# Kernel tuning notes

Hardware: AMD Instinct MI355X
Metric: run time of the kernel (lower is better)

Reference implementation:

```python
import jax, jax.numpy as jnp
import numpy as np

B, L, DIM = 4, 2048, 512
H, D = 8, 64
SCALE = D ** -0.5
NEG = -10000.0


def setup_inputs() -> dict:
    key = jax.random.key(0)
    ks = jax.random.split(key, 5)
    std = 1.0 / np.sqrt(DIM)
    return {
        "x": jax.random.normal(ks[0], (B, L, DIM), dtype=jnp.float32),
        "wq": jax.random.normal(ks[1], (H * D, DIM), dtype=jnp.float32) * std,
        "wk": jax.random.normal(ks[2], (H * D, DIM), dtype=jnp.float32) * std,
        "wv": jax.random.normal(ks[3], (H * D, DIM), dtype=jnp.float32) * std,
        "wo": jax.random.normal(ks[4], (DIM, H * D), dtype=jnp.float32) * std,
    }


def reference(x, wq, wk, wv, wo):
    b, l, _ = x.shape
    # projections (torch Linear: y = x @ W.T), split heads -> [b,h,l,d]
    q = (x @ wq.T).reshape(b, l, H, D).transpose(0, 2, 1, 3)
    k = (x @ wk.T).reshape(b, l, H, D).transpose(0, 2, 1, 3)
    v = (x @ wv.T).reshape(b, l, H, D).transpose(0, 2, 1, 3)
    scores = jnp.einsum("bhld,bhsd->bhls", q, k) * SCALE
    scores = jnp.nan_to_num(scores, nan=0.0, posinf=10000.0, neginf=NEG)
    diag = jnp.eye(l, dtype=bool)[None, None]  # [1,1,l,l]
    scores = jnp.where(diag, NEG, scores)
    attn = jax.nn.softmax(scores, axis=-1)
    attn = jnp.where(diag, 0.0, attn)
    attn = jnp.nan_to_num(attn, nan=0.0, posinf=0.0, neginf=0.0)
    out = jnp.einsum("bhls,bhsd->bhld", attn, v)
    out = out.transpose(0, 2, 1, 3).reshape(b, l, H * D)
    return out @ wo.T
```

## Files before the change

kernel.cpp:

```cpp
#include <hip/hip_runtime.h>
#include <hip/hip_bf16.h>


#define Bsz 4
#define Lsz 2048
#define DIMsz 512
#define Hsz 8
#define Dsz 64

typedef _Float16 f16;
typedef __attribute__((ext_vector_type(8))) _Float16 f16x8;
typedef __attribute__((ext_vector_type(4))) _Float16 f16x4;
typedef __attribute__((ext_vector_type(2))) __fp16 fp16x2;
typedef __attribute__((ext_vector_type(4))) float f32x4;
typedef unsigned int u32;

#if __has_builtin(__builtin_amdgcn_exp2f)
#define EXP2(x) __builtin_amdgcn_exp2f(x)
#else
#define EXP2(x) __expf(0.6931471805599453f * (x))
#endif

__device__ __forceinline__ u32 pack2(float a, float b) {
#if __has_builtin(__builtin_amdgcn_cvt_pkrtz)
    fp16x2 h = __builtin_amdgcn_cvt_pkrtz(a, b);
    return __builtin_bit_cast(u32, h);
#else
    fp16x2 h; h.x = (__fp16)a; h.y = (__fp16)b;
    return __builtin_bit_cast(u32, h);
#endif
}

__device__ __forceinline__ void gl2lds16(const void* g, void* l) {
    __builtin_amdgcn_global_load_lds(
        (const __attribute__((address_space(1))) u32*)g,
        (__attribute__((address_space(3))) u32*)l, 16, 0, 0);
}

__global__ __launch_bounds__(256) void pack_f16(
    const float* __restrict__ x, const float* __restrict__ wq,
    const float* __restrict__ wk, const float* __restrict__ wv,
    const float* __restrict__ wo,
    f16* __restrict__ xh, f16* __restrict__ w3h, f16* __restrict__ woh)
{
    const int seg = blockIdx.y;
    const float* s; f16* d; int n; float sc = 1.0f;
    switch (seg) {
        case 0: s = x;  d = xh;            n = 4194304; break;
        case 1: s = wq; d = w3h;           n = 262144; sc = 0.18033688011112042f; break;
        case 2: s = wk; d = w3h + 262144;  n = 262144; break;
        case 3: s = wv; d = w3h + 524288;  n = 262144; break;
        default: s = wo; d = woh;          n = 262144; break;
    }
    int i = (blockIdx.x * 256 + threadIdx.x) * 4;
    if (i >= n) return;
    float4 v = *(const float4*)(s + i);
    f16x4 o;
    o.x = (f16)(v.x * sc); o.y = (f16)(v.y * sc);
    o.z = (f16)(v.z * sc); o.w = (f16)(v.w * sc);
    *(f16x4*)(d + i) = o;
}

__global__ __launch_bounds__(256) void gemm_qkv_f16(
    const f16* __restrict__ A, const f16* __restrict__ B,
    f16* __restrict__ qh, f16* __restrict__ kh, f16* __restrict__ vth)
{
    __shared__ __align__(16) char smem[17408];
    f16* Ash = (f16*)smem;
    f16* Bsh = (f16*)(smem + 8192);

    const int tid = threadIdx.x;
    const int w = tid >> 6, lane = tid & 63;
    const int quad = lane >> 4, low = lane & 15;
    const int wm = w >> 1, wn = w & 1;
    const int m0 = blockIdx.y * 128, n0 = blockIdx.x * 128;

    f32x4 acc[4][4];
    #pragma unroll
    for (int i = 0; i < 4; i++)
        #pragma unroll
        for (int j = 0; j < 4; j++) acc[i][j] = (f32x4){0.f, 0.f, 0.f, 0.f};

    #pragma unroll 1
    for (int k0 = 0; k0 < DIMsz; k0 += 32) {
        __syncthreads();
        #pragma unroll
        for (int j = 0; j < 2; j++) {
            int t = j * 256 + tid;
            int r = t >> 2, g = t & 3;
            int gc = (g ^ ((r >> 1) & 3)) * 8;
            char* lb = (char*)Ash + (j * 256 + w * 64) * 16;
            gl2lds16(A + (size_t)(m0 + r) * DIMsz + k0 + gc, lb);
            char* lb2 = (char*)Bsh + (j * 256 + w * 64) * 16;
            gl2lds16(B + (size_t)(n0 + r) * DIMsz + k0 + gc, lb2);
        }
        __syncthreads();

        f16x8 af[4], bf[4];
        #pragma unroll
        for (int mt = 0; mt < 4; mt++) {
            int ar = wm * 64 + mt * 16 + low;
            af[mt] = *(const f16x8*)&Ash[ar * 32 + ((quad ^ ((ar >> 1) & 3)) << 3)];
        }
        #pragma unroll
        for (int nt = 0; nt < 4; nt++) {
            int br = wn * 64 + nt * 16 + low;
            bf[nt] = *(const f16x8*)&Bsh[br * 32 + ((quad ^ ((br >> 1) & 3)) << 3)];
        }
        #pragma unroll
        for (int mt = 0; mt < 4; mt++)
            #pragma unroll
            for (int nt = 0; nt < 4; nt++)
                acc[mt][nt] = __builtin_amdgcn_mfma_f32_16x16x32_f16(
                    af[mt], bf[nt], acc[mt][nt], 0, 0, 0);
    }

    const int proj = n0 >> 9;
    if (proj < 2) {
        f16* dst = (proj == 0) ? qh : kh;
        #pragma unroll
        for (int nt = 0; nt < 4; nt++) {
            int n = n0 + wn * 64 + nt * 16 + low;
            int c = n & 511, h = c >> 6, d = c & 63;
            #pragma unroll
            for (int mt = 0; mt < 4; mt++)
                #pragma unroll
                for (int r = 0; r < 4; r++) {
                    int m = m0 + wm * 64 + mt * 16 + quad * 4 + r;
                    int b_ = m >> 11, l = m & (Lsz - 1);
                    size_t bh = (size_t)(b_ * Hsz + h);
                    dst[(bh * Lsz + l) * Dsz + d] = (f16)acc[mt][nt][r];
                }
        }
    } else {
        const int hb = (n0 & 511) >> 6;
        f16* Tv = (f16*)smem;
        const int b_ = m0 >> 11, l0 = m0 & (Lsz - 1);
        #pragma unroll 1
        for (int hs = 0; hs < 2; hs++) {
            __syncthreads();
            if (wn == hs) {
                #pragma unroll
                for (int nt = 0; nt < 4; nt++) {
                    int d = nt * 16 + low;
                    #pragma unroll
                    for (int mt = 0; mt < 4; mt++)
                        #pragma unroll
                        for (int r = 0; r < 4; r++) {
                            int l = wm * 64 + mt * 16 + quad * 4 + r;
                            Tv[d * 136 + l] = (f16)acc[mt][nt][r];
                        }
                }
            }
            __syncthreads();
            int d = tid >> 2, seg = tid & 3;
            size_t bh = (size_t)(b_ * Hsz + hb + hs);
            f16* dstp = vth + (bh * 64 + d) * (size_t)Lsz + l0 + seg * 32;
            const f16* srcp = Tv + d * 136 + seg * 32;
            #pragma unroll
            for (int j = 0; j < 4; j++)
                *(f16x8*)(dstp + j * 8) = *(const f16x8*)(srcp + j * 8);
        }
    }
}

__global__ __launch_bounds__(256) void attn_mfma(
    const f16* __restrict__ q, const f16* __restrict__ k,
    const f16* __restrict__ vt, f16* __restrict__ ctx)
{
    __shared__ f16 Ks[64][72];
    __shared__ f16 Vs[64][72];
    __shared__ u32 Ppk[4][640];

    const int tid = threadIdx.x;
    const int w = tid >> 6, lane = tid & 63;
    const int quad = lane >> 4, low = lane & 15;
    const int bh = blockIdx.x;
    const int qb64 = blockIdx.y * 64;
    const int q0 = qb64 + w * 16;
    const size_t kvb = (size_t)bh * Lsz;

    f16x8 qf[2];
    #pragma unroll
    for (int ks = 0; ks < 2; ks++)
        qf[ks] = *(const f16x8*)(q + (kvb + q0 + low) * Dsz + ks * 32 + quad * 8);

    f32x4 acc[4];
    float lsum = 0.f;
    #pragma unroll
    for (int i = 0; i < 4; i++) acc[i] = (f32x4){0.f, 0.f, 0.f, 0.f};

    #pragma unroll 1
    for (int s0 = 0; s0 < Lsz; s0 += 64) {
        __syncthreads();
        {
            const f16x8* kg = (const f16x8*)(k + (kvb + s0) * Dsz);
            const f16x8* vg = (const f16x8*)(vt + ((size_t)bh << 17) + s0);
            #pragma unroll
            for (int i = 0; i < 2; i++) {
                int idx = i * 256 + tid;
                int r = idx >> 3, g = idx & 7;
                *(f16x8*)&Ks[r][g * 8] = kg[idx];
                *(f16x8*)&Vs[r][g * 8] = vg[r * 256 + g];
            }
        }
        __syncthreads();

        f32x4 st[4];
        #pragma unroll
        for (int nt = 0; nt < 4; nt++) {
            f16x8 k0 = *(const f16x8*)&Ks[nt * 16 + low][quad * 8];
            f16x8 k1 = *(const f16x8*)&Ks[nt * 16 + low][32 + quad * 8];
            f32x4 t = {0.f, 0.f, 0.f, 0.f};
            t = __builtin_amdgcn_mfma_f32_16x16x32_f16(k0, qf[0], t, 0, 0, 0);
            t = __builtin_amdgcn_mfma_f32_16x16x32_f16(k1, qf[1], t, 0, 0, 0);
            st[nt] = t;
        }

        #pragma unroll
        for (int nt = 0; nt < 4; nt++) {
            float p0 = EXP2(st[nt][0]), p1 = EXP2(st[nt][1]);
            float p2 = EXP2(st[nt][2]), p3 = EXP2(st[nt][3]);
            if (s0 == qb64 && nt == w) {
                p0 = (low == quad * 4 + 0) ? 0.f : p0;
                p1 = (low == quad * 4 + 1) ? 0.f : p1;
                p2 = (low == quad * 4 + 2) ? 0.f : p2;
                p3 = (low == quad * 4 + 3) ? 0.f : p3;
            }
            lsum += (p0 + p1) + (p2 + p3);
            int sp = nt * 8 + quad * 2;
            Ppk[w][sp * 20 + low]        = pack2(p0, p1);
            Ppk[w][(sp + 1) * 20 + low]  = pack2(p2, p3);
        }

        union { u32 u[4]; f16x8 v; } pf0, pf1;
        #pragma unroll
        for (int jj = 0; jj < 4; jj++) {
            pf0.u[jj] = Ppk[w][(quad * 4 + jj) * 20 + low];
            pf1.u[jj] = Ppk[w][(16 + quad * 4 + jj) * 20 + low];
        }

        #pragma unroll
        for (int dt = 0; dt < 4; dt++) {
            f16x8 v0 = *(const f16x8*)&Vs[dt * 16 + low][quad * 8];
            f16x8 v1 = *(const f16x8*)&Vs[dt * 16 + low][32 + quad * 8];
            f32x4 a = acc[dt];
            a = __builtin_amdgcn_mfma_f32_16x16x32_f16(v0, pf0.v, a, 0, 0, 0);
            a = __builtin_amdgcn_mfma_f32_16x16x32_f16(v1, pf1.v, a, 0, 0, 0);
            acc[dt] = a;
        }
    }

    lsum += __shfl_xor(lsum, 16);
    lsum += __shfl_xor(lsum, 32);
    const float inv = 1.0f / lsum;

    const int b = bh >> 3, h = bh & 7;
    f16* op = ctx + ((size_t)(b * Lsz + q0 + low)) * DIMsz + h * 64 + quad * 4;
    #pragma unroll
    for (int dt = 0; dt < 4; dt++) {
        f16x4 o;
        o.x = (f16)(acc[dt][0] * inv); o.y = (f16)(acc[dt][1] * inv);
        o.z = (f16)(acc[dt][2] * inv); o.w = (f16)(acc[dt][3] * inv);
        *(f16x4*)(op + dt * 16) = o;
    }
}

__global__ __launch_bounds__(256) void gemm_out_f16(
    const f16* __restrict__ A, const f16* __restrict__ B,
    float* __restrict__ C)
{
    __shared__ f16 Ash[64 * 32];
    __shared__ f16 Bsh[64 * 32];
    const int tid = threadIdx.x;
    const int w = tid >> 6, lane = tid & 63;
    const int quad = lane >> 4, low = lane & 15;
    const int wm = w >> 1, wn = w & 1;
    const int m0 = blockIdx.y * 64, n0 = blockIdx.x * 64;

    f32x4 acc[2][2];
    #pragma unroll
    for (int i = 0; i < 2; i++)
        #pragma unroll
        for (int j = 0; j < 2; j++) acc[i][j] = (f32x4){0.f, 0.f, 0.f, 0.f};

    #pragma unroll 1
    for (int k0 = 0; k0 < DIMsz; k0 += 32) {
        __syncthreads();
        {
            int r = tid >> 2, g = tid & 3;
            int gc = (g ^ ((r >> 1) & 3)) * 8;
            gl2lds16(A + (size_t)(m0 + r) * DIMsz + k0 + gc, (char*)Ash + w * 64 * 16);
            gl2lds16(B + (size_t)(n0 + r) * DIMsz + k0 + gc, (char*)Bsh + w * 64 * 16);
        }
        __syncthreads();

        f16x8 af[2], bf[2];
        #pragma unroll
        for (int mt = 0; mt < 2; mt++) {
            int ar = wm * 32 + mt * 16 + low;
            af[mt] = *(const f16x8*)&Ash[ar * 32 + ((quad ^ ((ar >> 1) & 3)) << 3)];
        }
        #pragma unroll
        for (int nt = 0; nt < 2; nt++) {
            int br = wn * 32 + nt * 16 + low;
            bf[nt] = *(const f16x8*)&Bsh[br * 32 + ((quad ^ ((br >> 1) & 3)) << 3)];
        }
        #pragma unroll
        for (int mt = 0; mt < 2; mt++)
            #pragma unroll
            for (int nt = 0; nt < 2; nt++)
                acc[mt][nt] = __builtin_amdgcn_mfma_f32_16x16x32_f16(
                    af[mt], bf[nt], acc[mt][nt], 0, 0, 0);
    }

    #pragma unroll
    for (int mt = 0; mt < 2; mt++)
        #pragma unroll
        for (int r = 0; r < 4; r++) {
            int m = m0 + wm * 32 + mt * 16 + quad * 4 + r;
            #pragma unroll
            for (int nt = 0; nt < 2; nt++) {
                int n = n0 + wn * 32 + nt * 16 + low;
                C[(size_t)m * DIMsz + n] = acc[mt][nt][r];
            }
        }
}

extern "C" void kernel_launch(void* const* d_in, const int* in_sizes, int n_in,
                              void* d_out, int out_size, void* d_ws, size_t ws_size,
                              hipStream_t stream) {
    const float* x  = (const float*)d_in[0];
    const float* wq = (const float*)d_in[1];
    const float* wk = (const float*)d_in[2];
    const float* wv = (const float*)d_in[3];
    const float* wo = (const float*)d_in[4];
    float* out = (float*)d_out;

    const size_t NTOK = (size_t)Bsz * Lsz;
    const size_t XSZ  = NTOK * DIMsz;

    f16* xh   = (f16*)d_ws;
    f16* w3h  = xh + XSZ;
    f16* woh  = w3h + 3 * 262144;
    f16* qh   = woh + 262144;
    f16* kh   = qh + XSZ;
    f16* vth  = kh + XSZ;
    f16* ctxh = vth + XSZ;

    dim3 gp(4096, 5);
    pack_f16<<<gp, 256, 0, stream>>>(x, wq, wk, wv, wo, xh, w3h, woh);

    dim3 g1(1536 / 128, NTOK / 128);
    gemm_qkv_f16<<<g1, 256, 0, stream>>>(xh, w3h, qh, kh, vth);

    dim3 g2(Bsz * Hsz, Lsz / 64);
    attn_mfma<<<g2, 256, 0, stream>>>(qh, kh, vth, ctxh);

    dim3 g3(DIMsz / 64, NTOK / 64);
    gemm_out_f16<<<g3, 256, 0, stream>>>(ctxh, woh, out);
}
```

Measured before the change: 188.7 us.

## Process two 16-row query tiles per wave in attention to reuse K/V fragments

Each wave in the attention kernel now handles 32 query rows as two 16-row MFMA tiles instead of one, so each block covers 128 queries and the grid's query dimension is halved. Every K and V fragment read from LDS now feeds two MFMAs, and the global K/V tile loads are shared by twice as many queries, cutting LDS and global traffic per unit of work. The P staging buffer is reshaped to hold both tiles and the diagonal mask logic is remapped to the new tiling. The cost is higher register pressure and only half as many blocks (512), which may reduce occupancy.

```diff
diff --git a/kernel.cpp b/kernel.cpp
--- a/kernel.cpp
+++ b/kernel.cpp
@@ -170,25 +170,38 @@
 {
     __shared__ f16 Ks[64][72];
     __shared__ f16 Vs[64][72];
-    __shared__ u32 Ppk[4][640];
+    __shared__ u32 Ppk[4][32][36];
 
     const int tid = threadIdx.x;
     const int w = tid >> 6, lane = tid & 63;
     const int quad = lane >> 4, low = lane & 15;
     const int bh = blockIdx.x;
-    const int qb64 = blockIdx.y * 64;
-    const int q0 = qb64 + w * 16;
+    const int qb = blockIdx.y;
+    const int q0 = qb * 128 + w * 32;
+    const int s0_diag = qb * 128 + (w & 2) * 32;
+    const int dnt0 = (w & 1) * 2;
     const size_t kvb = (size_t)bh * Lsz;
 
-    f16x8 qf[2];
-    #pragma unroll
-    for (int ks = 0; ks < 2; ks++)
-        qf[ks] = *(const f16x8*)(q + (kvb + q0 + low) * Dsz + ks * 32 + quad * 8);
-
-    f32x4 acc[4];
-    float lsum = 0.f;
-    #pragma unroll
-    for (int i = 0; i < 4; i++) acc[i] = (f32x4){0.f, 0.f, 0.f, 0.f};
+    f16x8 qf[2][2];
+    #pragma unroll
+    for (int qt = 0; qt < 2; qt++)
+        #pragma unroll
+        for (int ks = 0; ks < 2; ks++)
+            qf[qt][ks] = *(const f16x8*)(q + (kvb + q0 + qt * 16 + low) * Dsz
+                                           + ks * 32 + quad * 8);
+
+    f32x4 acc[2][4];
+    float lsum[2] = {0.f, 0.f};
+    #pragma unroll
+    for (int qt = 0; qt < 2; qt++)
+        #pragma unroll
+        for (int dt = 0; dt < 4; dt++) acc[qt][dt] = (f32x4){0.f, 0.f, 0.f, 0.f};
+
+    const f16* krow = &Ks[low][quad * 8];
+    const f16* vrow = &Vs[low][quad * 8];
+    u32* ppw = &Ppk[w][0][0];
+    const int pwb = quad * 2 * 36 + low;
+    const int prb = quad * 4 * 36 + low;
 
     #pragma unroll 1
     for (int s0 = 0; s0 < Lsz; s0 += 64) {
@@ -206,63 +219,80 @@
         }
         __syncthreads();
 
-        f32x4 st[4];
+        f32x4 st[4][2];
         #pragma unroll
         for (int nt = 0; nt < 4; nt++) {
-            f16x8 k0 = *(const f16x8*)&Ks[nt * 16 + low][quad * 8];
-            f16x8 k1 = *(const f16x8*)&Ks[nt * 16 + low][32 + quad * 8];
-            f32x4 t = {0.f, 0.f, 0.f, 0.f};
-            t = __builtin_amdgcn_mfma_f32_16x16x32_f16(k0, qf[0], t, 0, 0, 0);
-            t = __builtin_amdgcn_mfma_f32_16x16x32_f16(k1, qf[1], t, 0, 0, 0);
-            st[nt] = t;
-        }
-
-        #pragma unroll
-        for (int nt = 0; nt < 4; nt++) {
-            float p0 = EXP2(st[nt][0]), p1 = EXP2(st[nt][1]);
-            float p2 = EXP2(st[nt][2]), p3 = EXP2(st[nt][3]);
-            if (s0 == qb64 && nt == w) {
-                p0 = (low == quad * 4 + 0) ? 0.f : p0;
-                p1 = (low == quad * 4 + 1) ? 0.f : p1;
-                p2 = (low == quad * 4 + 2) ? 0.f : p2;
-                p3 = (low == quad * 4 + 3) ? 0.f : p3;
-            }
-            lsum += (p0 + p1) + (p2 + p3);
-            int sp = nt * 8 + quad * 2;
-            Ppk[w][sp * 20 + low]        = pack2(p0, p1);
-            Ppk[w][(sp + 1) * 20 + low]  = pack2(p2, p3);
-        }
-
-        union { u32 u[4]; f16x8 v; } pf0, pf1;
-        #pragma unroll
-        for (int jj = 0; jj < 4; jj++) {
-            pf0.u[jj] = Ppk[w][(quad * 4 + jj) * 20 + low];
-            pf1.u[jj] = Ppk[w][(16 + quad * 4 + jj) * 20 + low];
-        }
+            f16x8 k0 = *(const f16x8*)(krow + nt * 16 * 72);
+            f16x8 k1 = *(const f16x8*)(krow + nt * 16 * 72 + 32);
+            #pragma unroll
+            for (int qt = 0; qt < 2; qt++) {
+                f32x4 t = {0.f, 0.f, 0.f, 0.f};
+                t = __builtin_amdgcn_mfma_f32_16x16x32_f16(k0, qf[qt][0], t, 0, 0, 0);
+                t = __builtin_amdgcn_mfma_f32_16x16x32_f16(k1, qf[qt][1], t, 0, 0, 0);
+                st[nt][qt] = t;
+            }
+        }
+
+        const bool dchunk = (s0 == s0_diag);
+        #pragma unroll
+        for (int nt = 0; nt < 4; nt++)
+            #pragma unroll
+            for (int qt = 0; qt < 2; qt++) {
+                float p0 = EXP2(st[nt][qt][0]), p1 = EXP2(st[nt][qt][1]);
+                float p2 = EXP2(st[nt][qt][2]), p3 = EXP2(st[nt][qt][3]);
+                if (dchunk && nt == dnt0 + qt) {
+                    p0 = (low == quad * 4 + 0) ? 0.f : p0;
+                    p1 = (low == quad * 4 + 1) ? 0.f : p1;
+                    p2 = (low == quad * 4 + 2) ? 0.f : p2;
+                    p3 = (low == quad * 4 + 3) ? 0.f : p3;
+                }
+                lsum[qt] += (p0 + p1) + (p2 + p3);
+                ppw[pwb + (nt * 8 + 0) * 36 + qt * 16] = pack2(p0, p1);
+                ppw[pwb + (nt * 8 + 1) * 36 + qt * 16] = pack2(p2, p3);
+            }
+
+        union { u32 u[4]; f16x8 v; } pf[2][2];
+        #pragma unroll
+        for (int qt = 0; qt < 2; qt++)
+            #pragma unroll
+            for (int ks = 0; ks < 2; ks++)
+                #pragma unroll
+                for (int jj = 0; jj < 4; jj++)
+                    pf[qt][ks].u[jj] = ppw[prb + (ks * 16 + jj) * 36 + qt * 16];
 
         #pragma unroll
         for (int dt = 0; dt < 4; dt++) {
-            f16x8 v0 = *(const f16x8*)&Vs[dt * 16 + low][quad * 8];
-            f16x8 v1 = *(const f16x8*)&Vs[dt * 16 + low][32 + quad * 8];
-            f32x4 a = acc[dt];
-            a = __builtin_amdgcn_mfma_f32_16x16x32_f16(v0, pf0.v, a, 0, 0, 0);
-            a = __builtin_amdgcn_mfma_f32_16x16x32_f16(v1, pf1.v, a, 0, 0, 0);
-            acc[dt] = a;
-        }
-    }
-
-    lsum += __shfl_xor(lsum, 16);
-    lsum += __shfl_xor(lsum, 32);
-    const float inv = 1.0f / lsum;
+            f16x8 v0 = *(const f16x8*)(vrow + dt * 16 * 72);
+            f16x8 v1 = *(const f16x8*)(vrow + dt * 16 * 72 + 32);
+            #pragma unroll
+            for (int qt = 0; qt < 2; qt++) {
+                f32x4 a = acc[qt][dt];
+                a = __builtin_amdgcn_mfma_f32_16x16x32_f16(v0, pf[qt][0].v, a, 0, 0, 0);
+                a = __builtin_amdgcn_mfma_f32_16x16x32_f16(v1, pf[qt][1].v, a, 0, 0, 0);
+                acc[qt][dt] = a;
+            }
+        }
+    }
+
+    #pragma unroll
+    for (int qt = 0; qt < 2; qt++) {
+        lsum[qt] += __shfl_xor(lsum[qt], 16);
+        lsum[qt] += __shfl_xor(lsum[qt], 32);
+    }
 
     const int b = bh >> 3, h = bh & 7;
-    f16* op = ctx + ((size_t)(b * Lsz + q0 + low)) * DIMsz + h * 64 + quad * 4;
-    #pragma unroll
-    for (int dt = 0; dt < 4; dt++) {
-        f16x4 o;
-        o.x = (f16)(acc[dt][0] * inv); o.y = (f16)(acc[dt][1] * inv);
-        o.z = (f16)(acc[dt][2] * inv); o.w = (f16)(acc[dt][3] * inv);
-        *(f16x4*)(op + dt * 16) = o;
+    #pragma unroll
+    for (int qt = 0; qt < 2; qt++) {
+        const float inv = 1.0f / lsum[qt];
+        f16* op = ctx + ((size_t)(b * Lsz + q0 + qt * 16 + low)) * DIMsz
+                      + h * 64 + quad * 4;
+        #pragma unroll
+        for (int dt = 0; dt < 4; dt++) {
+            f16x4 o;
+            o.x = (f16)(acc[qt][dt][0] * inv); o.y = (f16)(acc[qt][dt][1] * inv);
+            o.z = (f16)(acc[qt][dt][2] * inv); o.w = (f16)(acc[qt][dt][3] * inv);
+            *(f16x4*)(op + dt * 16) = o;
+        }
     }
 }
 
@@ -354,7 +384,7 @@
     dim3 g1(1536 / 128, NTOK / 128);
     gemm_qkv_f16<<<g1, 256, 0, stream>>>(xh, w3h, qh, kh, vth);
 
-    dim3 g2(Bsz * Hsz, Lsz / 64);
+    dim3 g2(Bsz * Hsz, Lsz / 128);
     attn_mfma<<<g2, 256, 0, stream>>>(qh, kh, vth, ctxh);
 
     dim3 g3(DIMsz / 64, NTOK / 64);
```

Result: slower. 199.8 us (+5.9%).

## Restructure attention to 32x32x16 MFMA with split-KV warps and direct LDS loads

Applied to the files above, without the earlier changes.

Rewrites the attention kernel so each pair of warps shares a 32-query group and splits each 64-key tile between them. Scores and PV now use 32x32x16 MFMA instead of 16x16x32, and the partial outputs and row sums are combined through shared memory at the end. K/V tiles are loaded with global-to-LDS direct loads into XOR-swizzled layouts to avoid bank conflicts and register staging. The goal is fewer MFMA issues and less LDS traffic per FLOP, at the cost of an extra cross-warp reduction and more accumulator registers.

```diff
diff --git a/kernel.cpp b/kernel.cpp
--- a/kernel.cpp
+++ b/kernel.cpp
@@ -13,6 +13,7 @@
 typedef __attribute__((ext_vector_type(4))) _Float16 f16x4;
 typedef __attribute__((ext_vector_type(2))) __fp16 fp16x2;
 typedef __attribute__((ext_vector_type(4))) float f32x4;
+typedef __attribute__((ext_vector_type(16))) float f32x16;
 typedef unsigned int u32;
 
 #if __has_builtin(__builtin_amdgcn_exp2f)
@@ -168,101 +169,139 @@
     const f16* __restrict__ q, const f16* __restrict__ k,
     const f16* __restrict__ vt, f16* __restrict__ ctx)
 {
-    __shared__ f16 Ks[64][72];
-    __shared__ f16 Vs[64][72];
-    __shared__ u32 Ppk[4][640];
+    __shared__ __align__(16) char smem[16384];
+    __shared__ u32 Ppk[4][16][33];
+    __shared__ float Ls[2][32];
+
+    f16* Ks = (f16*)smem;
+    f16* Vs = (f16*)(smem + 8192);
 
     const int tid = threadIdx.x;
     const int w = tid >> 6, lane = tid & 63;
-    const int quad = lane >> 4, low = lane & 15;
+    const int col = lane & 31;
+    const int h = lane >> 5;
     const int bh = blockIdx.x;
-    const int qb64 = blockIdx.y * 64;
-    const int q0 = qb64 + w * 16;
+    const int qb = blockIdx.y;
+    const int grp = w >> 1;
+    const int kw = w & 1;
+    const int q0w = qb * 64 + grp * 32;
     const size_t kvb = (size_t)bh * Lsz;
 
-    f16x8 qf[2];
+    f16x8 qf[4];
     #pragma unroll
-    for (int ks = 0; ks < 2; ks++)
-        qf[ks] = *(const f16x8*)(q + (kvb + q0 + low) * Dsz + ks * 32 + quad * 8);
-
-    f32x4 acc[4];
+    for (int s = 0; s < 4; s++)
+        qf[s] = *(const f16x8*)(q + (kvb + q0w + col) * Dsz + s * 16 + h * 8);
+
+    f32x16 acc[2];
+    #pragma unroll
+    for (int dt = 0; dt < 2; dt++)
+        #pragma unroll
+        for (int i = 0; i < 16; i++) acc[dt][i] = 0.f;
     float lsum = 0.f;
-    #pragma unroll
-    for (int i = 0; i < 4; i++) acc[i] = (f32x4){0.f, 0.f, 0.f, 0.f};
 
     #pragma unroll 1
     for (int s0 = 0; s0 < Lsz; s0 += 64) {
         __syncthreads();
-        {
-            const f16x8* kg = (const f16x8*)(k + (kvb + s0) * Dsz);
-            const f16x8* vg = (const f16x8*)(vt + ((size_t)bh << 17) + s0);
-            #pragma unroll
-            for (int i = 0; i < 2; i++) {
-                int idx = i * 256 + tid;
-                int r = idx >> 3, g = idx & 7;
-                *(f16x8*)&Ks[r][g * 8] = kg[idx];
-                *(f16x8*)&Vs[r][g * 8] = vg[r * 256 + g];
-            }
-        }
-        __syncthreads();
-
-        f32x4 st[4];
-        #pragma unroll
-        for (int nt = 0; nt < 4; nt++) {
-            f16x8 k0 = *(const f16x8*)&Ks[nt * 16 + low][quad * 8];
-            f16x8 k1 = *(const f16x8*)&Ks[nt * 16 + low][32 + quad * 8];
-            f32x4 t = {0.f, 0.f, 0.f, 0.f};
-            t = __builtin_amdgcn_mfma_f32_16x16x32_f16(k0, qf[0], t, 0, 0, 0);
-            t = __builtin_amdgcn_mfma_f32_16x16x32_f16(k1, qf[1], t, 0, 0, 0);
-            st[nt] = t;
-        }
-
-        #pragma unroll
-        for (int nt = 0; nt < 4; nt++) {
-            float p0 = EXP2(st[nt][0]), p1 = EXP2(st[nt][1]);
-            float p2 = EXP2(st[nt][2]), p3 = EXP2(st[nt][3]);
-            if (s0 == qb64 && nt == w) {
-                p0 = (low == quad * 4 + 0) ? 0.f : p0;
-                p1 = (low == quad * 4 + 1) ? 0.f : p1;
-                p2 = (low == quad * 4 + 2) ? 0.f : p2;
-                p3 = (low == quad * 4 + 3) ? 0.f : p3;
-            }
-            lsum += (p0 + p1) + (p2 + p3);
-            int sp = nt * 8 + quad * 2;
-            Ppk[w][sp * 20 + low]        = pack2(p0, p1);
-            Ppk[w][(sp + 1) * 20 + low]  = pack2(p2, p3);
-        }
-
-        union { u32 u[4]; f16x8 v; } pf0, pf1;
-        #pragma unroll
-        for (int jj = 0; jj < 4; jj++) {
-            pf0.u[jj] = Ppk[w][(quad * 4 + jj) * 20 + low];
-            pf1.u[jj] = Ppk[w][(16 + quad * 4 + jj) * 20 + low];
-        }
-
-        #pragma unroll
-        for (int dt = 0; dt < 4; dt++) {
-            f16x8 v0 = *(const f16x8*)&Vs[dt * 16 + low][quad * 8];
-            f16x8 v1 = *(const f16x8*)&Vs[dt * 16 + low][32 + quad * 8];
-            f32x4 a = acc[dt];
-            a = __builtin_amdgcn_mfma_f32_16x16x32_f16(v0, pf0.v, a, 0, 0, 0);
-            a = __builtin_amdgcn_mfma_f32_16x16x32_f16(v1, pf1.v, a, 0, 0, 0);
-            acc[dt] = a;
-        }
-    }
-
-    lsum += __shfl_xor(lsum, 16);
+        #pragma unroll
+        for (int i = 0; i < 2; i++) {
+            int idx = i * 256 + tid;
+            int r = idx >> 3, g = idx & 7;
+            int gc = (g ^ (r & 7)) * 8;
+            char* kl = (char*)Ks + (i * 256 + w * 64) * 16;
+            char* vl = (char*)Vs + (i * 256 + w * 64) * 16;
+            gl2lds16(k + (kvb + s0 + r) * Dsz + gc, kl);
+            gl2lds16(vt + ((size_t)bh * Dsz + r) * Lsz + s0 + gc, vl);
+        }
+        __syncthreads();
+
+        f32x16 st;
+        #pragma unroll
+        for (int i = 0; i < 16; i++) st[i] = 0.f;
+        #pragma unroll
+        for (int s = 0; s < 4; s++) {
+            f16x8 kf = *(const f16x8*)(Ks + (kw * 32 + col) * 64 +
+                           (((s * 2 + h) ^ (col & 7)) << 3));
+            st = __builtin_amdgcn_mfma_f32_32x32x16_f16(kf, qf[s], st, 0, 0, 0);
+        }
+
+        float pv[16];
+        #pragma unroll
+        for (int i = 0; i < 16; i++) pv[i] = EXP2(st[i]);
+        if (s0 == qb * 64 && kw == grp) {
+            #pragma unroll
+            for (int i = 0; i < 16; i++) {
+                int row = (i & 3) + 8 * (i >> 2) + 4 * h;
+                pv[i] = (row == col) ? 0.f : pv[i];
+            }
+        }
+        #pragma unroll
+        for (int i = 0; i < 16; i++) lsum += pv[i];
+
+        #pragma unroll
+        for (int r4 = 0; r4 < 4; r4++) {
+            Ppk[w][h * 2 + 4 * r4][col]     = pack2(pv[4 * r4 + 0], pv[4 * r4 + 1]);
+            Ppk[w][h * 2 + 4 * r4 + 1][col] = pack2(pv[4 * r4 + 2], pv[4 * r4 + 3]);
+        }
+
+        union { u32 u[4]; f16x8 v; } pf[2];
+        #pragma unroll
+        for (int ks = 0; ks < 2; ks++)
+            #pragma unroll
+            for (int jj = 0; jj < 4; jj++)
+                pf[ks].u[jj] = Ppk[w][ks * 8 + h * 4 + jj][col];
+
+        #pragma unroll
+        for (int dt = 0; dt < 2; dt++)
+            #pragma unroll
+            for (int ks = 0; ks < 2; ks++) {
+                f16x8 vf = *(const f16x8*)(Vs + (dt * 32 + col) * 64 +
+                               (((kw * 4 + ks * 2 + h) ^ (col & 7)) << 3));
+                acc[dt] = __builtin_amdgcn_mfma_f32_32x32x16_f16(
+                    vf, pf[ks].v, acc[dt], 0, 0, 0);
+            }
+    }
+
     lsum += __shfl_xor(lsum, 32);
-    const float inv = 1.0f / lsum;
-
-    const int b = bh >> 3, h = bh & 7;
-    f16* op = ctx + ((size_t)(b * Lsz + q0 + low)) * DIMsz + h * 64 + quad * 4;
-    #pragma unroll
-    for (int dt = 0; dt < 4; dt++) {
-        f16x4 o;
-        o.x = (f16)(acc[dt][0] * inv); o.y = (f16)(acc[dt][1] * inv);
-        o.z = (f16)(acc[dt][2] * inv); o.w = (f16)(acc[dt][3] * inv);
-        *(f16x4*)(op + dt * 16) = o;
+
+    __syncthreads();
+    float* Om = (float*)smem;
+    if (kw == 1) {
+        float* og = Om + grp * 64 * 32;
+        #pragma unroll
+        for (int dt = 0; dt < 2; dt++)
+            #pragma unroll
+            for (int i = 0; i < 16; i++) {
+                int row = (i & 3) + 8 * (i >> 2) + 4 * h;
+                og[(dt * 32 + row) * 32 + col] = acc[dt][i];
+            }
+        if (h == 0) Ls[grp][col] = lsum;
+    }
+    __syncthreads();
+    if (kw == 0) {
+        const float* og = Om + grp * 64 * 32;
+        #pragma unroll
+        for (int dt = 0; dt < 2; dt++)
+            #pragma unroll
+            for (int i = 0; i < 16; i++) {
+                int row = (i & 3) + 8 * (i >> 2) + 4 * h;
+                acc[dt][i] += og[(dt * 32 + row) * 32 + col];
+            }
+        lsum += Ls[grp][col];
+        const float inv = 1.0f / lsum;
+
+        const int b = bh >> 3, hh = bh & 7;
+        f16* op = ctx + ((size_t)(b * Lsz + q0w + col)) * DIMsz + hh * 64;
+        #pragma unroll
+        for (int dt = 0; dt < 2; dt++)
+            #pragma unroll
+            for (int r4 = 0; r4 < 4; r4++) {
+                f16x4 o;
+                o.x = (f16)(acc[dt][4 * r4 + 0] * inv);
+                o.y = (f16)(acc[dt][4 * r4 + 1] * inv);
+                o.z = (f16)(acc[dt][4 * r4 + 2] * inv);
+                o.w = (f16)(acc[dt][4 * r4 + 3] * inv);
+                *(f16x4*)(op + dt * 32 + 8 * r4 + 4 * h) = o;
+            }
     }
 }
 
```

Result: faster. 180.1 us (-4.6%).
